# Kernel optimization log

Measured on AMD Instinct MI355X. Metric: run time of the kernel, lower is better.

The kernel has to match this reference:

```python
import jax, jax.numpy as jnp
import numpy as np

WIN_RAD = 1
EPS = 1e-07


def _window_inds(h, w):
    # Flattened pixel indices of every (2r+1)x(2r+1) sliding window -> [n_win, win_size]
    win_diam = 2 * WIN_RAD + 1
    r = jnp.arange(h - win_diam + 1)
    c = jnp.arange(w - win_diam + 1)
    dr = jnp.arange(win_diam)
    dc = jnp.arange(win_diam)
    rows = r[:, None, None, None] + dr[None, None, :, None]  # [H', 1, 3, 1]
    cols = c[None, :, None, None] + dc[None, None, None, :]  # [1, W', 1, 3]
    inds = rows * w + cols                                   # [H', W', 3, 3]
    return inds.reshape(-1, win_diam * win_diam)


def setup_inputs() -> dict:
    key = jax.random.key(0)
    k1, k2 = jax.random.split(key)
    target = jax.random.uniform(k1, (3, 512, 512), dtype=jnp.float32)
    style_map = jax.random.uniform(k2, (3, 512, 512), dtype=jnp.float32)
    return {"target": target, "style_map": style_map}


def reference(target, style_map):
    d, h, w = target.shape
    win_size = (2 * WIN_RAD + 1) ** 2  # 9

    win_inds = _window_inds(h, w)                  # [n_win, 9]
    ravel_img = target.reshape(d, h * w).T         # [hw, 3]
    winI = ravel_img[win_inds]                     # [n_win, 9, 3]

    win_mu = jnp.mean(winI, axis=1, keepdims=True)                     # [n_win, 1, 3]
    win_var = (jnp.einsum('nji,njk->nik', winI, winI) / win_size
               - jnp.einsum('nji,njk->nik', win_mu, win_mu))           # [n_win, 3, 3]
    inv = jnp.linalg.inv(win_var + (EPS / win_size) * jnp.eye(3, dtype=target.dtype))

    Xc = winI - win_mu                                                 # centered windows
    X = jnp.einsum('nij,njk->nik', Xc, inv)                            # [n_win, 9, 3]
    # Per-window Laplacian block: I - (1/win_size) * (1 + X Xc^T)
    vals = (jnp.eye(win_size, dtype=target.dtype)
            - (1.0 / win_size) * (1.0 + jnp.einsum('nij,nkj->nik', X, Xc)))  # [n_win, 9, 9]

    # trace(V L V^T) computed directly from window blocks (same math as the
    # explicit sparse COO assembly + sparse mm in the original module):
    # sum_n sum_{i,j} vals[n,i,j] * <V[:, win_inds[n,i]], V[:, win_inds[n,j]]>
    V = style_map.reshape(3, -1)            # [3, hw]
    Vw = V[:, win_inds]                     # [3, n_win, 9]
    t = jnp.einsum('nij,cnj->cni', vals, Vw)
    return jnp.sum(t * Vw)
```

## Files before the change

### kernel.cpp

```cpp
#include <hip/hip_runtime.h>

#define H 512
#define W 512
#define HW (H * W)
#define NW 510
#define NWIN (NW * NW)
#define EPS 1e-7f


__global__ __launch_bounds__(256)
void matting_quadform_kernel(const float* __restrict__ T,
                             const float* __restrict__ S,
                             float* __restrict__ out) {
    int idx = blockIdx.x * blockDim.x + threadIdx.x;
    float contrib = 0.0f;
    if (idx < NWIN) {
        int r = idx / NW;
        int c = idx - r * NW;

        float tv[3][9], sv[3][9];
        #pragma unroll
        for (int k = 0; k < 3; ++k) {
            const float* tb = T + k * HW + r * W + c;
            const float* sb = S + k * HW + r * W + c;
            #pragma unroll
            for (int dr = 0; dr < 3; ++dr) {
                #pragma unroll
                for (int dc = 0; dc < 3; ++dc) {
                    tv[k][dr * 3 + dc] = tb[dr * W + dc];
                    sv[k][dr * 3 + dc] = sb[dr * W + dc];
                }
            }
        }

        float s0 = 0, s1 = 0, s2 = 0;
        float G00 = 0, G01 = 0, G02 = 0, G11 = 0, G12 = 0, G22 = 0;
        #pragma unroll
        for (int j = 0; j < 9; ++j) {
            float a0 = tv[0][j], a1 = tv[1][j], a2 = tv[2][j];
            s0 += a0; s1 += a1; s2 += a2;
            G00 += a0 * a0; G01 += a0 * a1; G02 += a0 * a2;
            G11 += a1 * a1; G12 += a1 * a2; G22 += a2 * a2;
        }

        const float inv9 = 1.0f / 9.0f;
        float mu0 = s0 * inv9, mu1 = s1 * inv9, mu2 = s2 * inv9;
        const float reg = EPS * (1.0f / 9.0f);
        float c00 = G00 * inv9 - mu0 * mu0 + reg;
        float c01 = G01 * inv9 - mu0 * mu1;
        float c02 = G02 * inv9 - mu0 * mu2;
        float c11 = G11 * inv9 - mu1 * mu1 + reg;
        float c12 = G12 * inv9 - mu1 * mu2;
        float c22 = G22 * inv9 - mu2 * mu2 + reg;

        float d0 = c11 * c22 - c12 * c12;
        float d1 = c02 * c12 - c01 * c22;
        float d2 = c01 * c12 - c02 * c11;
        float det = c00 * d0 + c01 * d1 + c02 * d2;
        float idet = __fdividef(1.0f, det);
        float i00 = d0 * idet;
        float i01 = d1 * idet;
        float i02 = d2 * idet;
        float i11 = (c00 * c22 - c02 * c02) * idet;
        float i12 = (c01 * c02 - c00 * c12) * idet;
        float i22 = (c00 * c11 - c01 * c01) * idet;

        float acc = 0.0f;
        #pragma unroll
        for (int ch = 0; ch < 3; ++ch) {
            float sf = 0, qf = 0, y0f = 0, y1f = 0, y2f = 0;
            #pragma unroll
            for (int j = 0; j < 9; ++j) {
                float v = sv[ch][j];
                sf += v; qf += v * v;
                y0f += tv[0][j] * v;
                y1f += tv[1][j] * v;
                y2f += tv[2][j] * v;
            }
            float y0 = y0f - mu0 * sf;
            float y1 = y1f - mu1 * sf;
            float y2 = y2f - mu2 * sf;
            float quad = y0 * (i00 * y0 + i01 * y1 + i02 * y2)
                       + y1 * (i01 * y0 + i11 * y1 + i12 * y2)
                       + y2 * (i02 * y0 + i12 * y1 + i22 * y2);
            acc += qf - sf * sf * inv9 - quad * inv9;
        }
        contrib = acc;
    }

    #pragma unroll
    for (int off = 32; off > 0; off >>= 1)
        contrib += __shfl_down(contrib, off, 64);

    __shared__ float wsum[4];
    int lane = threadIdx.x & 63;
    int wid = threadIdx.x >> 6;
    if (lane == 0) wsum[wid] = contrib;
    __syncthreads();
    if (threadIdx.x == 0) {
        float b = wsum[0] + wsum[1] + wsum[2] + wsum[3];
        atomicAdd(out, b);
    }
}

extern "C" void kernel_launch(void* const* d_in, const int* in_sizes, int n_in,
                              void* d_out, int out_size, void* d_ws, size_t ws_size,
                              hipStream_t stream) {
    const float* T = (const float*)d_in[0];
    const float* S = (const float*)d_in[1];
    float* out = (float*)d_out;

    int blocks = (NWIN + 255) / 256;
    hipLaunchKernelGGL(matting_quadform_kernel, dim3(blocks), dim3(256), 0, stream,
                       T, S, out);
}
```

Baseline: 72.21 us.

## Process two adjacent windows per thread with vectorized float2 loads

Each thread now handles two horizontally adjacent 3x3 windows. It loads a 3x4 patch per channel with float2 vector loads and reuses the overlapping columns for both windows. This cuts redundant global loads and halves the thread count and per-thread reduction overhead. In exchange it uses more registers per thread (72 floats of patch data), which may lower occupancy. Since c is always even, the float2 accesses stay 8-byte aligned.

```diff
diff --git a/kernel.cpp b/kernel.cpp
--- a/kernel.cpp
+++ b/kernel.cpp
@@ -4,7 +4,8 @@
 #define W 512
 #define HW (H * W)
 #define NW 510
-#define NWIN (NW * NW)
+#define NPR 255
+#define NPAIR (NW * NPR)
 #define EPS 1e-7f
 
 
@@ -14,78 +15,93 @@
                              float* __restrict__ out) {
     int idx = blockIdx.x * blockDim.x + threadIdx.x;
     float contrib = 0.0f;
-    if (idx < NWIN) {
-        int r = idx / NW;
-        int c = idx - r * NW;
+    if (idx < NPAIR) {
+        int r = idx / NPR;
+        int c = (idx - r * NPR) * 2;
 
-        float tv[3][9], sv[3][9];
+        float tv[3][12], sv[3][12];
         #pragma unroll
         for (int k = 0; k < 3; ++k) {
             const float* tb = T + k * HW + r * W + c;
             const float* sb = S + k * HW + r * W + c;
             #pragma unroll
             for (int dr = 0; dr < 3; ++dr) {
-                #pragma unroll
-                for (int dc = 0; dc < 3; ++dc) {
-                    tv[k][dr * 3 + dc] = tb[dr * W + dc];
-                    sv[k][dr * 3 + dc] = sb[dr * W + dc];
-                }
+                const float2* tp = reinterpret_cast<const float2*>(tb + dr * W);
+                const float2* sp = reinterpret_cast<const float2*>(sb + dr * W);
+                float2 t0 = tp[0], t1 = tp[1];
+                float2 q0 = sp[0], q1 = sp[1];
+                tv[k][dr * 4 + 0] = t0.x; tv[k][dr * 4 + 1] = t0.y;
+                tv[k][dr * 4 + 2] = t1.x; tv[k][dr * 4 + 3] = t1.y;
+                sv[k][dr * 4 + 0] = q0.x; sv[k][dr * 4 + 1] = q0.y;
+                sv[k][dr * 4 + 2] = q1.x; sv[k][dr * 4 + 3] = q1.y;
             }
         }
 
-        float s0 = 0, s1 = 0, s2 = 0;
-        float G00 = 0, G01 = 0, G02 = 0, G11 = 0, G12 = 0, G22 = 0;
+        const float inv9 = 1.0f / 9.0f;
+        const float reg = EPS * (1.0f / 9.0f);
+
         #pragma unroll
-        for (int j = 0; j < 9; ++j) {
-            float a0 = tv[0][j], a1 = tv[1][j], a2 = tv[2][j];
-            s0 += a0; s1 += a1; s2 += a2;
-            G00 += a0 * a0; G01 += a0 * a1; G02 += a0 * a2;
-            G11 += a1 * a1; G12 += a1 * a2; G22 += a2 * a2;
+        for (int wofs = 0; wofs < 2; ++wofs) {
+            float s0 = 0, s1 = 0, s2 = 0;
+            float G00 = 0, G01 = 0, G02 = 0, G11 = 0, G12 = 0, G22 = 0;
+            #pragma unroll
+            for (int dr = 0; dr < 3; ++dr) {
+                #pragma unroll
+                for (int dc = 0; dc < 3; ++dc) {
+                    int j = dr * 4 + dc + wofs;
+                    float a0 = tv[0][j], a1 = tv[1][j], a2 = tv[2][j];
+                    s0 += a0; s1 += a1; s2 += a2;
+                    G00 += a0 * a0; G01 += a0 * a1; G02 += a0 * a2;
+                    G11 += a1 * a1; G12 += a1 * a2; G22 += a2 * a2;
+                }
+            }
+
+            float mu0 = s0 * inv9, mu1 = s1 * inv9, mu2 = s2 * inv9;
+            float c00 = G00 * inv9 - mu0 * mu0 + reg;
+            float c01 = G01 * inv9 - mu0 * mu1;
+            float c02 = G02 * inv9 - mu0 * mu2;
+            float c11 = G11 * inv9 - mu1 * mu1 + reg;
+            float c12 = G12 * inv9 - mu1 * mu2;
+            float c22 = G22 * inv9 - mu2 * mu2 + reg;
+
+            float d0 = c11 * c22 - c12 * c12;
+            float d1 = c02 * c12 - c01 * c22;
+            float d2 = c01 * c12 - c02 * c11;
+            float det = c00 * d0 + c01 * d1 + c02 * d2;
+            float idet = __fdividef(1.0f, det);
+            float i00 = d0 * idet;
+            float i01 = d1 * idet;
+            float i02 = d2 * idet;
+            float i11 = (c00 * c22 - c02 * c02) * idet;
+            float i12 = (c01 * c02 - c00 * c12) * idet;
+            float i22 = (c00 * c11 - c01 * c01) * idet;
+
+            float acc = 0.0f;
+            #pragma unroll
+            for (int ch = 0; ch < 3; ++ch) {
+                float sf = 0, qf = 0, y0f = 0, y1f = 0, y2f = 0;
+                #pragma unroll
+                for (int dr = 0; dr < 3; ++dr) {
+                    #pragma unroll
+                    for (int dc = 0; dc < 3; ++dc) {
+                        int j = dr * 4 + dc + wofs;
+                        float v = sv[ch][j];
+                        sf += v; qf += v * v;
+                        y0f += tv[0][j] * v;
+                        y1f += tv[1][j] * v;
+                        y2f += tv[2][j] * v;
+                    }
+                }
+                float y0 = y0f - mu0 * sf;
+                float y1 = y1f - mu1 * sf;
+                float y2 = y2f - mu2 * sf;
+                float quad = y0 * (i00 * y0 + i01 * y1 + i02 * y2)
+                           + y1 * (i01 * y0 + i11 * y1 + i12 * y2)
+                           + y2 * (i02 * y0 + i12 * y1 + i22 * y2);
+                acc += qf - sf * sf * inv9 - quad * inv9;
+            }
+            contrib += acc;
         }
-
-        const float inv9 = 1.0f / 9.0f;
-        float mu0 = s0 * inv9, mu1 = s1 * inv9, mu2 = s2 * inv9;
-        const float reg = EPS * (1.0f / 9.0f);
-        float c00 = G00 * inv9 - mu0 * mu0 + reg;
-        float c01 = G01 * inv9 - mu0 * mu1;
-        float c02 = G02 * inv9 - mu0 * mu2;
-        float c11 = G11 * inv9 - mu1 * mu1 + reg;
-        float c12 = G12 * inv9 - mu1 * mu2;
-        float c22 = G22 * inv9 - mu2 * mu2 + reg;
-
-        float d0 = c11 * c22 - c12 * c12;
-        float d1 = c02 * c12 - c01 * c22;
-        float d2 = c01 * c12 - c02 * c11;
-        float det = c00 * d0 + c01 * d1 + c02 * d2;
-        float idet = __fdividef(1.0f, det);
-        float i00 = d0 * idet;
-        float i01 = d1 * idet;
-        float i02 = d2 * idet;
-        float i11 = (c00 * c22 - c02 * c02) * idet;
-        float i12 = (c01 * c02 - c00 * c12) * idet;
-        float i22 = (c00 * c11 - c01 * c01) * idet;
-
-        float acc = 0.0f;
-        #pragma unroll
-        for (int ch = 0; ch < 3; ++ch) {
-            float sf = 0, qf = 0, y0f = 0, y1f = 0, y2f = 0;
-            #pragma unroll
-            for (int j = 0; j < 9; ++j) {
-                float v = sv[ch][j];
-                sf += v; qf += v * v;
-                y0f += tv[0][j] * v;
-                y1f += tv[1][j] * v;
-                y2f += tv[2][j] * v;
-            }
-            float y0 = y0f - mu0 * sf;
-            float y1 = y1f - mu1 * sf;
-            float y2 = y2f - mu2 * sf;
-            float quad = y0 * (i00 * y0 + i01 * y1 + i02 * y2)
-                       + y1 * (i01 * y0 + i11 * y1 + i12 * y2)
-                       + y2 * (i02 * y0 + i12 * y1 + i22 * y2);
-            acc += qf - sf * sf * inv9 - quad * inv9;
-        }
-        contrib = acc;
     }
 
     #pragma unroll
@@ -110,7 +126,7 @@
     const float* S = (const float*)d_in[1];
     float* out = (float*)d_out;
 
-    int blocks = (NWIN + 255) / 256;
+    int blocks = (NPAIR + 255) / 256;
     hipLaunchKernelGGL(matting_quadform_kernel, dim3(blocks), dim3(256), 0, stream,
                        T, S, out);
 }
```

Measured after the change: 66.78 us. 1.08x faster.
